# Kernel optimization log

Hardware: AMD Instinct MI355X
Metric: run time of the kernel (lower is better)

## Reference

```python
import jax, jax.numpy as jnp
import numpy as np

D, DPHI, HID, H = 256, 16, 128, 8

def setup_inputs() -> dict:
    key = jax.random.key(0)
    ks = jax.random.split(key, 24)
    s = 0.05
    inp = {
        "R_t": jax.random.normal(ks[0], (2, 128, D), dtype=jnp.float32),
        "R_ctx": jax.random.normal(ks[1], (2, 512, D), dtype=jnp.float32),
        "phi_t": jax.random.normal(ks[2], (2, 128, DPHI), dtype=jnp.float32),
        "phi_c": jax.random.normal(ks[3], (2, 512, DPHI), dtype=jnp.float32),
        "mask": jnp.ones((2, 512), dtype=bool),
        # params (torch Linear convention: y = x @ W.T + b)
        "Wq_w": jax.random.normal(ks[4], (D, D), dtype=jnp.float32) * s,
        "Wq_b": jnp.zeros((D,), dtype=jnp.float32),
        "kc_w": jax.random.normal(ks[5], (D, D), dtype=jnp.float32) * s,
        "kt_w": jax.random.normal(ks[6], (D, D), dtype=jnp.float32) * s,
        "kp1_w": jax.random.normal(ks[7], (HID, DPHI), dtype=jnp.float32) * s,
        "kp1_b": jnp.zeros((HID,), dtype=jnp.float32),
        "kp2_w": jax.random.normal(ks[8], (D, HID), dtype=jnp.float32) * s,
        "kp2_b": jnp.zeros((D,), dtype=jnp.float32),
        "vc_w": jax.random.normal(ks[9], (D, D), dtype=jnp.float32) * s,
        "vt_w": jax.random.normal(ks[10], (D, D), dtype=jnp.float32) * s,
        "vp1_w": jax.random.normal(ks[11], (HID, DPHI), dtype=jnp.float32) * s,
        "vp1_b": jnp.zeros((HID,), dtype=jnp.float32),
        "vp2_w": jax.random.normal(ks[12], (D, HID), dtype=jnp.float32) * s,
        "vp2_b": jnp.zeros((D,), dtype=jnp.float32),
        "g_w": jax.random.normal(ks[13], (D, 3 * D), dtype=jnp.float32) * s,
        "g_b": jnp.zeros((D,), dtype=jnp.float32),
        "out_w": jax.random.normal(ks[14], (D, D), dtype=jnp.float32) * s,
        "out_b": jnp.zeros((D,), dtype=jnp.float32),
    }
    return inp


def reference(R_t, R_ctx, phi_t, phi_c, mask,
              Wq_w, Wq_b, kc_w, kt_w, kp1_w, kp1_b, kp2_w, kp2_b,
              vc_w, vt_w, vp1_w, vp1_b, vp2_w, vp2_b,
              g_w, g_b, out_w, out_b):
    B, Nt, d = R_t.shape
    Nc = R_ctx.shape[1]
    dk = d // H
    # pairwise phi deltas: (B, Nt, Nc, d_phi)
    dphi = phi_t[:, :, None, :] - phi_c[:, None, :, :]
    # K = k_ctx(Rc) + k_tgt(Rt) + k_phi(dphi), broadcast instead of expand
    kphi = jax.nn.relu(dphi @ kp1_w.T + kp1_b) @ kp2_w.T + kp2_b
    K = (R_ctx @ kc_w.T)[:, None, :, :] + (R_t @ kt_w.T)[:, :, None, :] + kphi
    vphi = jax.nn.relu(dphi @ vp1_w.T + vp1_b) @ vp2_w.T + vp2_b
    V = (R_ctx @ vc_w.T)[:, None, :, :] + (R_t @ vt_w.T)[:, :, None, :] + vphi
    # gate on cat([K, V, |K-V|]) -- split gate weight to avoid concat
    gw1, gw2, gw3 = jnp.split(g_w, 3, axis=1)
    g = jax.nn.sigmoid(K @ gw1.T + V @ gw2.T + jnp.abs(K - V) @ gw3.T + g_b)
    Kg = K * g
    Vg = V * g
    # queries: (B, Nt, H, dk)
    Q = (R_t @ Wq_w.T + Wq_b).reshape(B, Nt, H, dk)
    Kh = Kg.reshape(B, Nt, Nc, H, dk)
    Vh = Vg.reshape(B, Nt, Nc, H, dk)
    scores = jnp.einsum('bnhd,bnchd->bhnc', Q, Kh) / jnp.sqrt(jnp.float32(dk))
    scores = jnp.where(mask[:, None, None, :], scores, -jnp.inf)
    attn = jax.nn.softmax(scores, axis=-1)
    ctx = jnp.einsum('bhnc,bnchd->bnhd', attn, Vh).reshape(B, Nt, d)
    return ctx @ out_w.T + out_b
```

## Files before the change

### kernel.cpp

```cpp
#include <hip/hip_runtime.h>
#include <hip/hip_bf16.h>
#include <stdint.h>


typedef __attribute__((ext_vector_type(8))) short short8;
typedef __attribute__((ext_vector_type(4))) float f32x4;

#define MFMA16(a, b, c) __builtin_amdgcn_mfma_f32_16x16x32_bf16(a, b, c, 0, 0, 0)
#define SPLIT 8

__device__ __forceinline__ short f2bf(float f) {
  union { float f; uint32_t u; } v; v.f = f;
  uint32_t u = v.u;
  u = (u + 0x7FFFu + ((u >> 16) & 1u)) >> 16;
  return (short)u;
}
__device__ __forceinline__ float bf2f(short s) {
  union { uint32_t u; float f; } v;
  v.u = ((uint32_t)(uint16_t)s) << 16;
  return v.f;
}

__device__ __forceinline__ int kvIdx(int r, int d) {
  return (r << 8) + ((((d >> 3) ^ (r & 7)) << 3) | (d & 7));
}
__device__ __forceinline__ int hIdx(int r, int hc) {
  return (r << 7) + ((((hc >> 3) ^ (r & 7)) << 3) | (hc & 7));
}

__global__ void prep_bf16(const float* __restrict__ kp1_w, const float* __restrict__ kp2_w,
                          const float* __restrict__ vp1_w, const float* __restrict__ vp2_w,
                          const float* __restrict__ g_w,
                          short* __restrict__ kp1b, short* __restrict__ kp2b,
                          short* __restrict__ vp1b, short* __restrict__ vp2b,
                          short* __restrict__ gw1b, short* __restrict__ gw2b,
                          short* __restrict__ gw3b) {
  int i = blockIdx.x * 256 + threadIdx.x;
  if (i < 2048) {
    kp1b[i] = f2bf(kp1_w[i]);
  } else if (i < 34816) {
    int j = i - 2048; kp2b[j] = f2bf(kp2_w[j]);
  } else if (i < 36864) {
    int j = i - 34816; vp1b[j] = f2bf(vp1_w[j]);
  } else if (i < 69632) {
    int j = i - 36864; vp2b[j] = f2bf(vp2_w[j]);
  } else if (i < 266240) {
    int j = i - 69632;
    int mat = j >> 16;
    int jj = j & 65535;
    int nrow = jj >> 8;
    int kcol = jj & 255;
    short v = f2bf(g_w[nrow * 768 + mat * 256 + kcol]);
    if (mat == 0) gw1b[jj] = v; else if (mat == 1) gw2b[jj] = v; else gw3b[jj] = v;
  }
}

__global__ void prep_gemm(const float* __restrict__ R_t, const float* __restrict__ R_ctx,
                          const float* __restrict__ Wq_w, const float* __restrict__ Wq_b,
                          const float* __restrict__ kc_w, const float* __restrict__ kt_w,
                          const float* __restrict__ kp2_b,
                          const float* __restrict__ vc_w, const float* __restrict__ vt_w,
                          const float* __restrict__ vp2_b,
                          float* __restrict__ Kc, float* __restrict__ Vc,
                          float* __restrict__ KtB, float* __restrict__ VtB,
                          float* __restrict__ Qs) {
  __shared__ __align__(16) float xr[8][256];
  int blk = blockIdx.x, t = threadIdx.x;
  const float* X; const float* W; float* O;
  float bias = 0.f, scale = 1.f;
  int r0;
  if (blk < 128)       { r0 = blk * 8;         X = R_ctx; W = kc_w; O = Kc; }
  else if (blk < 256)  { r0 = (blk - 128) * 8; X = R_ctx; W = vc_w; O = Vc; }
  else if (blk < 288)  { r0 = (blk - 256) * 8; X = R_t;   W = kt_w; O = KtB; bias = kp2_b[t]; }
  else if (blk < 320)  { r0 = (blk - 288) * 8; X = R_t;   W = vt_w; O = VtB; bias = vp2_b[t]; }
  else                 { r0 = (blk - 320) * 8; X = R_t;   W = Wq_w; O = Qs;  bias = Wq_b[t];
                         scale = 0.17677669529663689f; }
#pragma unroll
  for (int i = 0; i < 8; ++i) xr[i][t] = X[(r0 + i) * 256 + t];
  __syncthreads();
  const float* wr = &W[t * 256];
  float acc[8];
#pragma unroll
  for (int i = 0; i < 8; ++i) acc[i] = bias;
#pragma unroll 4
  for (int k = 0; k < 256; ++k) {
    float wv = wr[k];
#pragma unroll
    for (int i = 0; i < 8; ++i) acc[i] += xr[i][k] * wv;
  }
#pragma unroll
  for (int i = 0; i < 8; ++i) O[(r0 + i) * 256 + t] = acc[i] * scale;
}

__launch_bounds__(512, 2)
__global__ void taca_main(const float* __restrict__ phi_t, const float* __restrict__ phi_c,
                          const short* __restrict__ kp1b_, const short* __restrict__ kp2b_,
                          const short* __restrict__ vp1b_, const short* __restrict__ vp2b_,
                          const short* __restrict__ gw1b_, const short* __restrict__ gw2b_,
                          const short* __restrict__ gw3b_,
                          const float* __restrict__ kp1_b, const float* __restrict__ vp1_b,
                          const float* __restrict__ g_b,
                          const float* __restrict__ Kc, const float* __restrict__ Vc,
                          const float* __restrict__ KtB, const float* __restrict__ VtB,
                          const float* __restrict__ Qs,
                          float* __restrict__ mP, float* __restrict__ lP,
                          float* __restrict__ ctxP) {
  extern __shared__ __align__(16) short lds[];

  const int tid = threadIdx.x;
  const int w = tid >> 6;
  const int lane = tid & 63;
  const int q = lane >> 4;
  const int m15 = lane & 15;
  const int blk = blockIdx.x;
  const int s = blk & (SPLIT - 1);
  const int bn = blk >> 3;
  const int b = bn >> 7;

  float KtB_reg[2], VtB_reg[2], gb_reg[2];
#pragma unroll
  for (int nt = 0; nt < 2; ++nt) {
    int d = (w << 5) + (nt << 4) + m15;
    KtB_reg[nt] = KtB[(bn << 8) + d];
    VtB_reg[nt] = VtB[(bn << 8) + d];
    gb_reg[nt]  = g_b[d];
  }
  float kb_reg, vb_reg;
  {
    int hc = (w << 4) + m15;
    kb_reg = kp1_b[hc];
    vb_reg = vp1_b[hc];
  }
  short8 bQ;
  {
    const float* qp = &Qs[(bn << 8) + (w << 5) + (q << 3)];
    float4 x = *(const float4*)qp;
    float4 y = *(const float4*)(qp + 4);
    short8 z;
    z[0] = f2bf(x.x); z[1] = f2bf(x.y); z[2] = f2bf(x.z); z[3] = f2bf(x.w);
    z[4] = f2bf(y.x); z[5] = f2bf(y.y); z[6] = f2bf(y.z); z[7] = f2bf(y.w);
    bQ = z;
  }
  float pt[8] = {0, 0, 0, 0, 0, 0, 0, 0};
  if (q < 2) {
    const float* p = &phi_t[bn * 16 + (q << 3)];
    float4 x = *(const float4*)p;
    float4 y = *(const float4*)(p + 4);
    pt[0] = x.x; pt[1] = x.y; pt[2] = x.z; pt[3] = x.w;
    pt[4] = y.x; pt[5] = y.y; pt[6] = y.z; pt[7] = y.w;
  }
  short8 bHk, bHv;
  {
    int nr = (w << 4) + m15;
    short8 zk = {0, 0, 0, 0, 0, 0, 0, 0};
    short8 zv = {0, 0, 0, 0, 0, 0, 0, 0};
    if (q < 2) {
      zk = *(const short8*)&kp1b_[nr * 16 + (q << 3)];
      zv = *(const short8*)&vp1b_[nr * 16 + (q << 3)];
    }
    bHk = zk; bHv = zv;
  }

  const f32x4 zf = {0.f, 0.f, 0.f, 0.f};

  short8 aPhi[2][2];
#pragma unroll
  for (int ch = 0; ch < 2; ++ch)
#pragma unroll
    for (int Mt = 0; Mt < 2; ++Mt) {
      short8 z = {0, 0, 0, 0, 0, 0, 0, 0};
      if (q < 2) {
        int r = (s << 6) + (ch << 5) + (Mt << 4) + m15;
        const float* p = &phi_c[(((b << 9) + r) << 4) + (q << 3)];
        float4 x = *(const float4*)p;
        float4 y = *(const float4*)(p + 4);
        z[0] = f2bf(pt[0] - x.x); z[1] = f2bf(pt[1] - x.y);
        z[2] = f2bf(pt[2] - x.z); z[3] = f2bf(pt[3] - x.w);
        z[4] = f2bf(pt[4] - y.x); z[5] = f2bf(pt[5] - y.y);
        z[6] = f2bf(pt[6] - y.z); z[7] = f2bf(pt[7] - y.w);
      }
      aPhi[ch][Mt] = z;
    }

#pragma unroll
  for (int ch = 0; ch < 2; ++ch) {
    short* Hk = lds + 49152 + ch * 8192;
    short* Hv = Hk + 4096;
    f32x4 hk[2], hv[2];
#pragma unroll
    for (int Mt = 0; Mt < 2; ++Mt) {
      hk[Mt] = MFMA16(aPhi[ch][Mt], bHk, zf);
      hv[Mt] = MFMA16(aPhi[ch][Mt], bHv, zf);
    }
    int hc = (w << 4) + m15;
#pragma unroll
    for (int Mt = 0; Mt < 2; ++Mt)
#pragma unroll
      for (int i = 0; i < 4; ++i) {
        int hoff = hIdx((Mt << 4) + (q << 2) + i, hc);
        float hkv = hk[Mt][i] + kb_reg;
        Hk[hoff] = f2bf(hkv > 0.f ? hkv : 0.f);
        float hvv = hv[Mt][i] + vb_reg;
        Hv[hoff] = f2bf(hvv > 0.f ? hvv : 0.f);
      }
  }
  __syncthreads();

  for (int ch = 0; ch < 2; ++ch) {
    const int c0 = (s << 6) + (ch << 5);
    for (int kv = 0; kv < 2; ++kv) {
      const short* p2 = kv ? vp2b_ : kp2b_;
      const float* Cm = kv ? Vc : Kc;
      const short* Hsrc = lds + 49152 + ch * 8192 + kv * 4096;
      short* dst = lds + ch * 24576 + kv * 8192;
      short* Atile = lds + ch * 24576 + 16384;

      f32x4 accP[2][2];
#pragma unroll
      for (int Mt = 0; Mt < 2; ++Mt)
#pragma unroll
        for (int nt = 0; nt < 2; ++nt) {
          int d = (w << 5) + (nt << 4) + m15;
          float tbv = kv ? VtB_reg[nt] : KtB_reg[nt];
          f32x4 ci;
#pragma unroll
          for (int i = 0; i < 4; ++i) {
            int rl = (Mt << 4) + (q << 2) + i;
            ci[i] = Cm[((b << 9) + c0 + rl) * 256 + d] + tbv;
          }
          accP[Mt][nt] = ci;
        }

#pragma unroll
      for (int ks = 0; ks < 4; ++ks) {
        short8 aH[2];
#pragma unroll
        for (int Mt = 0; Mt < 2; ++Mt)
          aH[Mt] = *(const short8*)&Hsrc[hIdx((Mt << 4) + m15, (ks << 5) + (q << 3))];
#pragma unroll
        for (int nt = 0; nt < 2; ++nt) {
          int nd = (w << 5) + (nt << 4) + m15;
          short8 bb = *(const short8*)&p2[nd * 128 + (ks << 5) + (q << 3)];
#pragma unroll
          for (int Mt = 0; Mt < 2; ++Mt)
            accP[Mt][nt] = MFMA16(aH[Mt], bb, accP[Mt][nt]);
        }
      }

#pragma unroll
      for (int Mt = 0; Mt < 2; ++Mt)
#pragma unroll
        for (int nt = 0; nt < 2; ++nt) {
          int d = (w << 5) + (nt << 4) + m15;
#pragma unroll
          for (int i = 0; i < 4; ++i) {
            int rl = (Mt << 4) + (q << 2) + i;
            int off = kvIdx(rl, d);
            short sv = f2bf(accP[Mt][nt][i]);
            dst[off] = sv;
            if (kv) {
              float dd = bf2f((lds + ch * 24576)[off]) - bf2f(sv);
              Atile[off] = f2bf(__builtin_fabsf(dd));
            }
          }
        }
    }
  }
  __syncthreads();

  f32x4 accG[2][2][2];
#pragma unroll
  for (int ch = 0; ch < 2; ++ch)
#pragma unroll
    for (int Mt = 0; Mt < 2; ++Mt)
#pragma unroll
      for (int nt = 0; nt < 2; ++nt) accG[ch][Mt][nt] = zf;
#pragma unroll 2
  for (int ks = 0; ks < 8; ++ks) {
    short8 aK[2][2], aV[2][2], aA[2][2];
#pragma unroll
    for (int ch = 0; ch < 2; ++ch) {
      const short* Kt = lds + ch * 24576;
#pragma unroll
      for (int Mt = 0; Mt < 2; ++Mt) {
        int off = kvIdx((Mt << 4) + m15, (ks << 5) + (q << 3));
        aK[ch][Mt] = *(const short8*)&Kt[off];
        aV[ch][Mt] = *(const short8*)&Kt[off + 8192];
        aA[ch][Mt] = *(const short8*)&Kt[off + 16384];
      }
    }
#pragma unroll
    for (int nt = 0; nt < 2; ++nt) {
      int nd = (w << 5) + (nt << 4) + m15;
      int ko = (ks << 5) + (q << 3);
      short8 b1 = *(const short8*)&gw1b_[(nd << 8) + ko];
      short8 b2 = *(const short8*)&gw2b_[(nd << 8) + ko];
      short8 b3 = *(const short8*)&gw3b_[(nd << 8) + ko];
#pragma unroll
      for (int ch = 0; ch < 2; ++ch)
#pragma unroll
        for (int Mt = 0; Mt < 2; ++Mt) {
          accG[ch][Mt][nt] = MFMA16(aA[ch][Mt], b3, accG[ch][Mt][nt]);
          accG[ch][Mt][nt] = MFMA16(aV[ch][Mt], b2, accG[ch][Mt][nt]);
          accG[ch][Mt][nt] = MFMA16(aK[ch][Mt], b1, accG[ch][Mt][nt]);
        }
    }
  }
  __syncthreads();

#pragma unroll
  for (int ch = 0; ch < 2; ++ch) {
    short* Kt = lds + ch * 24576;
#pragma unroll
    for (int Mt = 0; Mt < 2; ++Mt)
#pragma unroll
      for (int nt = 0; nt < 2; ++nt)
#pragma unroll
        for (int i = 0; i < 4; ++i) {
          float z = accG[ch][Mt][nt][i] + gb_reg[nt];
          float g = 1.f / (1.f + __expf(-z));
          accG[ch][Mt][nt][i] = g;
          int off = kvIdx((Mt << 4) + (q << 2) + i, (w << 5) + (nt << 4) + m15);
          Kt[off] = f2bf(bf2f(Kt[off]) * g);
        }
  }
  asm volatile("s_waitcnt lgkmcnt(0)" ::: "memory");

  {
    f32x4 sc[2][2];
#pragma unroll
    for (int ch = 0; ch < 2; ++ch) {
      const short* Kt = lds + ch * 24576;
#pragma unroll
      for (int Mt = 0; Mt < 2; ++Mt) {
        short8 aKg = *(const short8*)&Kt[kvIdx((Mt << 4) + m15, (w << 5) + (q << 3))];
        sc[ch][Mt] = MFMA16(aKg, bQ, zf);
      }
    }
    float mx = -1e30f;
#pragma unroll
    for (int ch = 0; ch < 2; ++ch)
#pragma unroll
      for (int Mt = 0; Mt < 2; ++Mt)
#pragma unroll
        for (int i = 0; i < 4; ++i) mx = fmaxf(mx, sc[ch][Mt][i]);
    mx = fmaxf(mx, __shfl_xor(mx, 16));
    mx = fmaxf(mx, __shfl_xor(mx, 32));
    float pv[2][2][4];
    float ls = 0.f;
#pragma unroll
    for (int ch = 0; ch < 2; ++ch)
#pragma unroll
      for (int Mt = 0; Mt < 2; ++Mt)
#pragma unroll
        for (int i = 0; i < 4; ++i) {
          float e = __expf(sc[ch][Mt][i] - mx);
          pv[ch][Mt][i] = e;
          ls += e;
        }
    float ctxA[2] = {0.f, 0.f};
#pragma unroll
    for (int ntl = 0; ntl < 2; ++ntl) {
      int d = (w << 5) + (ntl << 4) + m15;
      float acc = 0.f;
#pragma unroll
      for (int ch = 0; ch < 2; ++ch) {
        const short* Vt = lds + ch * 24576 + 8192;
#pragma unroll
        for (int Mt = 0; Mt < 2; ++Mt)
#pragma unroll
          for (int i = 0; i < 4; ++i) {
            float vv = bf2f(Vt[kvIdx((Mt << 4) + (q << 2) + i, d)]);
            acc += pv[ch][Mt][i] * accG[ch][Mt][ntl][i] * vv;
          }
      }
      ctxA[ntl] = acc;
    }
    float l = ls;
    l += __shfl_xor(l, 16);
    l += __shfl_xor(l, 32);
#pragma unroll
    for (int ntl = 0; ntl < 2; ++ntl) {
      float cv = ctxA[ntl];
      cv += __shfl_xor(cv, 16);
      cv += __shfl_xor(cv, 32);
      if (q == 0)
        ctxP[(blk << 8) + (w << 5) + (ntl << 4) + m15] = cv;
    }
    if (q == 0 && m15 == 0) {
      mP[(blk << 3) + w] = mx;
      lP[(blk << 3) + w] = l;
    }
  }
}

__global__ void taca_merge(const float* __restrict__ mP, const float* __restrict__ lP,
                           const float* __restrict__ ctxP,
                           const float* __restrict__ out_w, const float* __restrict__ out_b,
                           float* __restrict__ out) {
  __shared__ __align__(16) float ctxbuf[256];
  const int bn = blockIdx.x;
  const int t = threadIdx.x;
  const int h = t >> 5;
  float mmax = -1e30f;
#pragma unroll
  for (int s = 0; s < SPLIT; ++s)
    mmax = fmaxf(mmax, mP[(((bn << 3) + s) << 3) + h]);
  float lsum = 0.f, csum = 0.f;
#pragma unroll
  for (int s = 0; s < SPLIT; ++s) {
    int idx = (bn << 3) + s;
    float e = __expf(mP[(idx << 3) + h] - mmax);
    lsum += lP[(idx << 3) + h] * e;
    csum += ctxP[(idx << 8) + t] * e;
  }
  ctxbuf[t] = csum / lsum;
  __syncthreads();
  float acc = out_b[t];
  const float* wr = &out_w[t << 8];
  float sacc = 0.f;
#pragma unroll 8
  for (int dd = 0; dd < 256; dd += 4) {
    float4 cvec = *(const float4*)&ctxbuf[dd];
    float4 wvec = *(const float4*)&wr[dd];
    sacc += cvec.x * wvec.x + cvec.y * wvec.y + cvec.z * wvec.z + cvec.w * wvec.w;
  }
  out[(bn << 8) + t] = acc + sacc;
}

extern "C" void kernel_launch(void* const* d_in, const int* in_sizes, int n_in,
                              void* d_out, int out_size, void* d_ws, size_t ws_size,
                              hipStream_t stream) {
  (void)in_sizes; (void)n_in; (void)out_size; (void)ws_size;
  const float* R_t   = (const float*)d_in[0];
  const float* R_ctx = (const float*)d_in[1];
  const float* phi_t = (const float*)d_in[2];
  const float* phi_c = (const float*)d_in[3];
  const float* Wq_w  = (const float*)d_in[5];
  const float* Wq_b  = (const float*)d_in[6];
  const float* kc_w  = (const float*)d_in[7];
  const float* kt_w  = (const float*)d_in[8];
  const float* kp1_w = (const float*)d_in[9];
  const float* kp1_b = (const float*)d_in[10];
  const float* kp2_w = (const float*)d_in[11];
  const float* kp2_b = (const float*)d_in[12];
  const float* vc_w  = (const float*)d_in[13];
  const float* vt_w  = (const float*)d_in[14];
  const float* vp1_w = (const float*)d_in[15];
  const float* vp1_b = (const float*)d_in[16];
  const float* vp2_w = (const float*)d_in[17];
  const float* vp2_b = (const float*)d_in[18];
  const float* g_w   = (const float*)d_in[19];
  const float* g_b   = (const float*)d_in[20];
  const float* out_w = (const float*)d_in[21];
  const float* out_b = (const float*)d_in[22];

  char* ws = (char*)d_ws;
  short* kp1b = (short*)(ws + 0);
  short* kp2b = (short*)(ws + 4096);
  short* vp1b = (short*)(ws + 69632);
  short* vp2b = (short*)(ws + 73728);
  short* gw1b = (short*)(ws + 139264);
  short* gw2b = (short*)(ws + 270336);
  short* gw3b = (short*)(ws + 401408);
  float* Kc   = (float*)(ws + 532480);
  float* Vc   = (float*)(ws + 1581056);
  float* KtB  = (float*)(ws + 2629632);
  float* VtB  = (float*)(ws + 2891776);
  float* Qs   = (float*)(ws + 3153920);
  float* mP   = (float*)(ws + 3416064);
  float* lP   = (float*)(ws + 3481600);
  float* ctxP = (float*)(ws + 3547136);

  static bool lds_attr_set = false;
  if (!lds_attr_set) {
    (void)hipFuncSetAttribute((const void*)taca_main,
                              hipFuncAttributeMaxDynamicSharedMemorySize, 131072);
    lds_attr_set = true;
  }

  prep_bf16<<<1040, 256, 0, stream>>>(kp1_w, kp2_w, vp1_w, vp2_w, g_w,
                                      kp1b, kp2b, vp1b, vp2b, gw1b, gw2b, gw3b);
  prep_gemm<<<352, 256, 0, stream>>>(R_t, R_ctx, Wq_w, Wq_b, kc_w, kt_w, kp2_b,
                                     vc_w, vt_w, vp2_b, Kc, Vc, KtB, VtB, Qs);
  taca_main<<<256 * SPLIT, 512, 131072, stream>>>(phi_t, phi_c, kp1b, kp2b, vp1b, vp2b,
                                                  gw1b, gw2b, gw3b, kp1_b, vp1_b, g_b,
                                                  Kc, Vc, KtB, VtB, Qs, mP, lP, ctxP);
  taca_merge<<<256, 256, 0, stream>>>(mP, lP, ctxP, out_w, out_b, (float*)d_out);
}
```

Before: 331.8 us.

## Double context split to shrink per-block tile and LDS for occupancy

Raises the context split from 8 to 16, so each block handles 32 context rows instead of 64. The per-block LDS falls from 128KB dynamic to 64KB static, and each wave holds half as many MFMA accumulator tiles. The aim is more resident blocks per CU and lower register pressure. In exchange, blocks double and so does the per-block fixed work (Q, bias and weight fragment loads, gate weight streaming), and the merge kernel reduces twice as many partials.

```diff
diff --git a/kernel.cpp b/kernel.cpp
--- a/kernel.cpp
+++ b/kernel.cpp
@@ -7,7 +7,7 @@
 typedef __attribute__((ext_vector_type(4))) float f32x4;
 
 #define MFMA16(a, b, c) __builtin_amdgcn_mfma_f32_16x16x32_bf16(a, b, c, 0, 0, 0)
-#define SPLIT 8
+#define SPLIT 16
 
 __device__ __forceinline__ short f2bf(float f) {
   union { float f; uint32_t u; } v; v.f = f;
@@ -105,7 +105,7 @@
                           const float* __restrict__ Qs,
                           float* __restrict__ mP, float* __restrict__ lP,
                           float* __restrict__ ctxP) {
-  extern __shared__ __align__(16) short lds[];
+  __shared__ __align__(16) short lds[32768];
 
   const int tid = threadIdx.x;
   const int w = tid >> 6;
@@ -114,7 +114,7 @@
   const int m15 = lane & 15;
   const int blk = blockIdx.x;
   const int s = blk & (SPLIT - 1);
-  const int bn = blk >> 3;
+  const int bn = blk >> 4;
   const int b = bn >> 7;
 
   float KtB_reg[2], VtB_reg[2], gb_reg[2];
@@ -163,131 +163,108 @@
 
   const f32x4 zf = {0.f, 0.f, 0.f, 0.f};
 
-  short8 aPhi[2][2];
-#pragma unroll
-  for (int ch = 0; ch < 2; ++ch)
-#pragma unroll
-    for (int Mt = 0; Mt < 2; ++Mt) {
-      short8 z = {0, 0, 0, 0, 0, 0, 0, 0};
-      if (q < 2) {
-        int r = (s << 6) + (ch << 5) + (Mt << 4) + m15;
-        const float* p = &phi_c[(((b << 9) + r) << 4) + (q << 3)];
-        float4 x = *(const float4*)p;
-        float4 y = *(const float4*)(p + 4);
-        z[0] = f2bf(pt[0] - x.x); z[1] = f2bf(pt[1] - x.y);
-        z[2] = f2bf(pt[2] - x.z); z[3] = f2bf(pt[3] - x.w);
-        z[4] = f2bf(pt[4] - y.x); z[5] = f2bf(pt[5] - y.y);
-        z[6] = f2bf(pt[6] - y.z); z[7] = f2bf(pt[7] - y.w);
-      }
-      aPhi[ch][Mt] = z;
-    }
-
+  short8 aPhi[2];
 #pragma unroll
   for (int ch = 0; ch < 2; ++ch) {
-    short* Hk = lds + 49152 + ch * 8192;
-    short* Hv = Hk + 4096;
-    f32x4 hk[2], hv[2];
-#pragma unroll
-    for (int Mt = 0; Mt < 2; ++Mt) {
-      hk[Mt] = MFMA16(aPhi[ch][Mt], bHk, zf);
-      hv[Mt] = MFMA16(aPhi[ch][Mt], bHv, zf);
-    }
+    short8 z = {0, 0, 0, 0, 0, 0, 0, 0};
+    if (q < 2) {
+      int r = (s << 5) + (ch << 4) + m15;
+      const float* p = &phi_c[(((b << 9) + r) << 4) + (q << 3)];
+      float4 x = *(const float4*)p;
+      float4 y = *(const float4*)(p + 4);
+      z[0] = f2bf(pt[0] - x.x); z[1] = f2bf(pt[1] - x.y);
+      z[2] = f2bf(pt[2] - x.z); z[3] = f2bf(pt[3] - x.w);
+      z[4] = f2bf(pt[4] - y.x); z[5] = f2bf(pt[5] - y.y);
+      z[6] = f2bf(pt[6] - y.z); z[7] = f2bf(pt[7] - y.w);
+    }
+    aPhi[ch] = z;
+  }
+
+#pragma unroll
+  for (int ch = 0; ch < 2; ++ch) {
+    short* Hk = lds + 24576 + ch * 4096;
+    short* Hv = Hk + 2048;
+    f32x4 hk = MFMA16(aPhi[ch], bHk, zf);
+    f32x4 hv = MFMA16(aPhi[ch], bHv, zf);
     int hc = (w << 4) + m15;
 #pragma unroll
-    for (int Mt = 0; Mt < 2; ++Mt)
-#pragma unroll
-      for (int i = 0; i < 4; ++i) {
-        int hoff = hIdx((Mt << 4) + (q << 2) + i, hc);
-        float hkv = hk[Mt][i] + kb_reg;
-        Hk[hoff] = f2bf(hkv > 0.f ? hkv : 0.f);
-        float hvv = hv[Mt][i] + vb_reg;
-        Hv[hoff] = f2bf(hvv > 0.f ? hvv : 0.f);
-      }
+    for (int i = 0; i < 4; ++i) {
+      int hoff = hIdx((q << 2) + i, hc);
+      float hkv = hk[i] + kb_reg;
+      Hk[hoff] = f2bf(hkv > 0.f ? hkv : 0.f);
+      float hvv = hv[i] + vb_reg;
+      Hv[hoff] = f2bf(hvv > 0.f ? hvv : 0.f);
+    }
   }
   __syncthreads();
 
   for (int ch = 0; ch < 2; ++ch) {
-    const int c0 = (s << 6) + (ch << 5);
+    const int c0 = (s << 5) + (ch << 4);
     for (int kv = 0; kv < 2; ++kv) {
       const short* p2 = kv ? vp2b_ : kp2b_;
       const float* Cm = kv ? Vc : Kc;
-      const short* Hsrc = lds + 49152 + ch * 8192 + kv * 4096;
-      short* dst = lds + ch * 24576 + kv * 8192;
-      short* Atile = lds + ch * 24576 + 16384;
-
-      f32x4 accP[2][2];
-#pragma unroll
-      for (int Mt = 0; Mt < 2; ++Mt)
-#pragma unroll
-        for (int nt = 0; nt < 2; ++nt) {
-          int d = (w << 5) + (nt << 4) + m15;
-          float tbv = kv ? VtB_reg[nt] : KtB_reg[nt];
-          f32x4 ci;
-#pragma unroll
-          for (int i = 0; i < 4; ++i) {
-            int rl = (Mt << 4) + (q << 2) + i;
-            ci[i] = Cm[((b << 9) + c0 + rl) * 256 + d] + tbv;
-          }
-          accP[Mt][nt] = ci;
+      const short* Hsrc = lds + 24576 + ch * 4096 + kv * 2048;
+      short* dst = lds + ch * 12288 + kv * 4096;
+      short* Atile = lds + ch * 12288 + 8192;
+
+      f32x4 accP[2];
+#pragma unroll
+      for (int nt = 0; nt < 2; ++nt) {
+        int d = (w << 5) + (nt << 4) + m15;
+        float tbv = kv ? VtB_reg[nt] : KtB_reg[nt];
+        f32x4 ci;
+#pragma unroll
+        for (int i = 0; i < 4; ++i) {
+          int rl = (q << 2) + i;
+          ci[i] = Cm[((b << 9) + c0 + rl) * 256 + d] + tbv;
         }
+        accP[nt] = ci;
+      }
 
 #pragma unroll
       for (int ks = 0; ks < 4; ++ks) {
-        short8 aH[2];
-#pragma unroll
-        for (int Mt = 0; Mt < 2; ++Mt)
-          aH[Mt] = *(const short8*)&Hsrc[hIdx((Mt << 4) + m15, (ks << 5) + (q << 3))];
+        short8 aH = *(const short8*)&Hsrc[hIdx(m15, (ks << 5) + (q << 3))];
 #pragma unroll
         for (int nt = 0; nt < 2; ++nt) {
           int nd = (w << 5) + (nt << 4) + m15;
           short8 bb = *(const short8*)&p2[nd * 128 + (ks << 5) + (q << 3)];
-#pragma unroll
-          for (int Mt = 0; Mt < 2; ++Mt)
-            accP[Mt][nt] = MFMA16(aH[Mt], bb, accP[Mt][nt]);
+          accP[nt] = MFMA16(aH, bb, accP[nt]);
         }
       }
 
 #pragma unroll
-      for (int Mt = 0; Mt < 2; ++Mt)
-#pragma unroll
-        for (int nt = 0; nt < 2; ++nt) {
-          int d = (w << 5) + (nt << 4) + m15;
-#pragma unroll
-          for (int i = 0; i < 4; ++i) {
-            int rl = (Mt << 4) + (q << 2) + i;
-            int off = kvIdx(rl, d);
-            short sv = f2bf(accP[Mt][nt][i]);
-            dst[off] = sv;
-            if (kv) {
-              float dd = bf2f((lds + ch * 24576)[off]) - bf2f(sv);
-              Atile[off] = f2bf(__builtin_fabsf(dd));
-            }
+      for (int nt = 0; nt < 2; ++nt) {
+        int d = (w << 5) + (nt << 4) + m15;
+#pragma unroll
+        for (int i = 0; i < 4; ++i) {
+          int off = kvIdx((q << 2) + i, d);
+          short sv = f2bf(accP[nt][i]);
+          dst[off] = sv;
+          if (kv) {
+            float dd = bf2f((lds + ch * 12288)[off]) - bf2f(sv);
+            Atile[off] = f2bf(__builtin_fabsf(dd));
           }
         }
+      }
     }
   }
   __syncthreads();
 
-  f32x4 accG[2][2][2];
+  f32x4 accG[2][2];
 #pragma unroll
   for (int ch = 0; ch < 2; ++ch)
 #pragma unroll
-    for (int Mt = 0; Mt < 2; ++Mt)
-#pragma unroll
-      for (int nt = 0; nt < 2; ++nt) accG[ch][Mt][nt] = zf;
+    for (int nt = 0; nt < 2; ++nt) accG[ch][nt] = zf;
 #pragma unroll 2
   for (int ks = 0; ks < 8; ++ks) {
-    short8 aK[2][2], aV[2][2], aA[2][2];
+    short8 aK[2], aV[2], aA[2];
 #pragma unroll
     for (int ch = 0; ch < 2; ++ch) {
-      const short* Kt = lds + ch * 24576;
-#pragma unroll
-      for (int Mt = 0; Mt < 2; ++Mt) {
-        int off = kvIdx((Mt << 4) + m15, (ks << 5) + (q << 3));
-        aK[ch][Mt] = *(const short8*)&Kt[off];
-        aV[ch][Mt] = *(const short8*)&Kt[off + 8192];
-        aA[ch][Mt] = *(const short8*)&Kt[off + 16384];
-      }
+      const short* Kt = lds + ch * 12288;
+      int off = kvIdx(m15, (ks << 5) + (q << 3));
+      aK[ch] = *(const short8*)&Kt[off];
+      aV[ch] = *(const short8*)&Kt[off + 4096];
+      aA[ch] = *(const short8*)&Kt[off + 8192];
     }
 #pragma unroll
     for (int nt = 0; nt < 2; ++nt) {
@@ -297,67 +274,56 @@
       short8 b2 = *(const short8*)&gw2b_[(nd << 8) + ko];
       short8 b3 = *(const short8*)&gw3b_[(nd << 8) + ko];
 #pragma unroll
-      for (int ch = 0; ch < 2; ++ch)
-#pragma unroll
-        for (int Mt = 0; Mt < 2; ++Mt) {
-          accG[ch][Mt][nt] = MFMA16(aA[ch][Mt], b3, accG[ch][Mt][nt]);
-          accG[ch][Mt][nt] = MFMA16(aV[ch][Mt], b2, accG[ch][Mt][nt]);
-          accG[ch][Mt][nt] = MFMA16(aK[ch][Mt], b1, accG[ch][Mt][nt]);
-        }
+      for (int ch = 0; ch < 2; ++ch) {
+        accG[ch][nt] = MFMA16(aA[ch], b3, accG[ch][nt]);
+        accG[ch][nt] = MFMA16(aV[ch], b2, accG[ch][nt]);
+        accG[ch][nt] = MFMA16(aK[ch], b1, accG[ch][nt]);
+      }
     }
   }
   __syncthreads();
 
 #pragma unroll
   for (int ch = 0; ch < 2; ++ch) {
-    short* Kt = lds + ch * 24576;
-#pragma unroll
-    for (int Mt = 0; Mt < 2; ++Mt)
-#pragma unroll
-      for (int nt = 0; nt < 2; ++nt)
-#pragma unroll
-        for (int i = 0; i < 4; ++i) {
-          float z = accG[ch][Mt][nt][i] + gb_reg[nt];
-          float g = 1.f / (1.f + __expf(-z));
-          accG[ch][Mt][nt][i] = g;
-          int off = kvIdx((Mt << 4) + (q << 2) + i, (w << 5) + (nt << 4) + m15);
-          Kt[off] = f2bf(bf2f(Kt[off]) * g);
-        }
+    short* Kt = lds + ch * 12288;
+#pragma unroll
+    for (int nt = 0; nt < 2; ++nt)
+#pragma unroll
+      for (int i = 0; i < 4; ++i) {
+        float z = accG[ch][nt][i] + gb_reg[nt];
+        float g = 1.f / (1.f + __expf(-z));
+        accG[ch][nt][i] = g;
+        int off = kvIdx((q << 2) + i, (w << 5) + (nt << 4) + m15);
+        Kt[off] = f2bf(bf2f(Kt[off]) * g);
+      }
   }
   asm volatile("s_waitcnt lgkmcnt(0)" ::: "memory");
 
   {
-    f32x4 sc[2][2];
+    f32x4 sc[2];
 #pragma unroll
     for (int ch = 0; ch < 2; ++ch) {
-      const short* Kt = lds + ch * 24576;
-#pragma unroll
-      for (int Mt = 0; Mt < 2; ++Mt) {
-        short8 aKg = *(const short8*)&Kt[kvIdx((Mt << 4) + m15, (w << 5) + (q << 3))];
-        sc[ch][Mt] = MFMA16(aKg, bQ, zf);
-      }
+      const short* Kt = lds + ch * 12288;
+      short8 aKg = *(const short8*)&Kt[kvIdx(m15, (w << 5) + (q << 3))];
+      sc[ch] = MFMA16(aKg, bQ, zf);
     }
     float mx = -1e30f;
 #pragma unroll
     for (int ch = 0; ch < 2; ++ch)
 #pragma unroll
-      for (int Mt = 0; Mt < 2; ++Mt)
-#pragma unroll
-        for (int i = 0; i < 4; ++i) mx = fmaxf(mx, sc[ch][Mt][i]);
+      for (int i = 0; i < 4; ++i) mx = fmaxf(mx, sc[ch][i]);
     mx = fmaxf(mx, __shfl_xor(mx, 16));
     mx = fmaxf(mx, __shfl_xor(mx, 32));
-    float pv[2][2][4];
+    float pv[2][4];
     float ls = 0.f;
 #pragma unroll
     for (int ch = 0; ch < 2; ++ch)
 #pragma unroll
-      for (int Mt = 0; Mt < 2; ++Mt)
-#pragma unroll
-        for (int i = 0; i < 4; ++i) {
-          float e = __expf(sc[ch][Mt][i] - mx);
-          pv[ch][Mt][i] = e;
-          ls += e;
-        }
+      for (int i = 0; i < 4; ++i) {
+        float e = __expf(sc[ch][i] - mx);
+        pv[ch][i] = e;
+        ls += e;
+      }
     float ctxA[2] = {0.f, 0.f};
 #pragma unroll
     for (int ntl = 0; ntl < 2; ++ntl) {
@@ -365,14 +331,12 @@
       float acc = 0.f;
 #pragma unroll
       for (int ch = 0; ch < 2; ++ch) {
-        const short* Vt = lds + ch * 24576 + 8192;
-#pragma unroll
-        for (int Mt = 0; Mt < 2; ++Mt)
-#pragma unroll
-          for (int i = 0; i < 4; ++i) {
-            float vv = bf2f(Vt[kvIdx((Mt << 4) + (q << 2) + i, d)]);
-            acc += pv[ch][Mt][i] * accG[ch][Mt][ntl][i] * vv;
-          }
+        const short* Vt = lds + ch * 12288 + 4096;
+#pragma unroll
+        for (int i = 0; i < 4; ++i) {
+          float vv = bf2f(Vt[kvIdx((q << 2) + i, d)]);
+          acc += pv[ch][i] * accG[ch][ntl][i] * vv;
+        }
       }
       ctxA[ntl] = acc;
     }
@@ -405,11 +369,11 @@
   float mmax = -1e30f;
 #pragma unroll
   for (int s = 0; s < SPLIT; ++s)
-    mmax = fmaxf(mmax, mP[(((bn << 3) + s) << 3) + h]);
+    mmax = fmaxf(mmax, mP[(((bn << 4) + s) << 3) + h]);
   float lsum = 0.f, csum = 0.f;
 #pragma unroll
   for (int s = 0; s < SPLIT; ++s) {
-    int idx = (bn << 3) + s;
+    int idx = (bn << 4) + s;
     float e = __expf(mP[(idx << 3) + h] - mmax);
     lsum += lP[(idx << 3) + h] * e;
     csum += ctxP[(idx << 8) + t] * e;
@@ -469,22 +433,15 @@
   float* VtB  = (float*)(ws + 2891776);
   float* Qs   = (float*)(ws + 3153920);
   float* mP   = (float*)(ws + 3416064);
-  float* lP   = (float*)(ws + 3481600);
-  float* ctxP = (float*)(ws + 3547136);
-
-  static bool lds_attr_set = false;
-  if (!lds_attr_set) {
-    (void)hipFuncSetAttribute((const void*)taca_main,
-                              hipFuncAttributeMaxDynamicSharedMemorySize, 131072);
-    lds_attr_set = true;
-  }
+  float* lP   = (float*)(ws + 3547136);
+  float* ctxP = (float*)(ws + 3678208);
 
   prep_bf16<<<1040, 256, 0, stream>>>(kp1_w, kp2_w, vp1_w, vp2_w, g_w,
                                       kp1b, kp2b, vp1b, vp2b, gw1b, gw2b, gw3b);
   prep_gemm<<<352, 256, 0, stream>>>(R_t, R_ctx, Wq_w, Wq_b, kc_w, kt_w, kp2_b,
                                      vc_w, vt_w, vp2_b, Kc, Vc, KtB, VtB, Qs);
-  taca_main<<<256 * SPLIT, 512, 131072, stream>>>(phi_t, phi_c, kp1b, kp2b, vp1b, vp2b,
-                                                  gw1b, gw2b, gw3b, kp1_b, vp1_b, g_b,
-                                                  Kc, Vc, KtB, VtB, Qs, mP, lP, ctxP);
+  taca_main<<<256 * SPLIT, 512, 0, stream>>>(phi_t, phi_c, kp1b, kp2b, vp1b, vp2b,
+                                             gw1b, gw2b, gw3b, kp1_b, vp1_b, g_b,
+                                             Kc, Vc, KtB, VtB, Qs, mP, lP, ctxP);
   taca_merge<<<256, 256, 0, stream>>>(mP, lP, ctxP, out_w, out_b, (float*)d_out);
 }
```

Measured after the change: 454.1 us. 1.37x slower.
